# Optimization experiments

Measured on AMD Instinct MI355X. Metric: run time of the kernel, lower is better.

The kernel has to match this reference:

```python
import math
import jax, jax.numpy as jnp
import numpy as np

D_MODEL = 512
NHEAD = 8
D_HEAD = D_MODEL // NHEAD
ATTN_TEMP = 1.0
B, LQ, LK = 2, 2048, 4096


def _linear_params(key, d_in, d_out):
    kw, kb = jax.random.split(key)
    bound = 1.0 / math.sqrt(d_in)
    W = jax.random.uniform(kw, (d_out, d_in), jnp.float32, -bound, bound)
    b = jax.random.uniform(kb, (d_out,), jnp.float32, -bound, bound)
    return W, b


def setup_inputs() -> dict:
    key = jax.random.key(0)
    ks = jax.random.split(key, 8)
    q = jax.random.normal(ks[0], (B, LQ, D_MODEL), jnp.float32)
    kv = jax.random.normal(ks[1], (B, LK, D_MODEL), jnp.float32)
    key_gate = jax.random.uniform(ks[2], (B, LK), jnp.float32)
    key_mask = jax.random.randint(ks[3], (B, LK), 0, 2, jnp.int32)
    Wq, bq = _linear_params(ks[4], D_MODEL, D_MODEL)
    Wk, bk = _linear_params(ks[5], D_MODEL, D_MODEL)
    Wv, bv = _linear_params(ks[6], D_MODEL, D_MODEL)
    Wo, bo = _linear_params(ks[7], D_MODEL, D_MODEL)
    return {"q": q, "kv": kv, "key_gate": key_gate, "key_mask": key_mask,
            "Wq": Wq, "bq": bq, "Wk": Wk, "bk": bk,
            "Wv": Wv, "bv": bv, "Wo": Wo, "bo": bo}


def reference(q, kv, key_gate, key_mask, Wq, bq, Wk, bk, Wv, bv, Wo, bo):
    Bq, Lq, _ = q.shape
    _, Lk, _ = kv.shape
    # projections -> (B, H, L, Dh)
    qp = (q @ Wq.T + bq).reshape(Bq, Lq, NHEAD, D_HEAD).transpose(0, 2, 1, 3)
    kp = (kv @ Wk.T + bk).reshape(Bq, Lk, NHEAD, D_HEAD).transpose(0, 2, 1, 3)
    vp = (kv @ Wv.T + bv).reshape(Bq, Lk, NHEAD, D_HEAD).transpose(0, 2, 1, 3)
    # scores: (B, H, Lq, Lk)
    scores = jnp.einsum('bhqd,bhkd->bhqk', qp, kp) / (math.sqrt(D_HEAD) * ATTN_TEMP)
    log_gate = jnp.log(jnp.clip(key_gate, 1e-6, None))  # (B, Lk)
    scores = scores + log_gate[:, None, None, :]
    pad = (key_mask == 0)[:, None, None, :]
    scores = jnp.where(pad, -jnp.inf, scores)
    attn = jax.nn.softmax(scores, axis=-1)  # dropout is identity in eval
    out = jnp.einsum('bhqk,bhkd->bhqd', attn, vp)
    out = out.transpose(0, 2, 1, 3).reshape(Bq, Lq, D_MODEL)
    return out @ Wo.T + bo
```

## Files before the change

kernel.cpp:

```cpp
#include <hip/hip_runtime.h>
#include <hip/hip_bf16.h>


using bf16  = __hip_bfloat16;
using bf16x8 = __attribute__((ext_vector_type(8))) short;
using f32x4  = __attribute__((ext_vector_type(4))) float;

#define MFMA16(a, b, c) __builtin_amdgcn_mfma_f32_16x16x32_bf16((a), (b), (c), 0, 0, 0)

#define SCALE_LOG2E 0.18033688011112042f

__device__ __forceinline__ bf16x8 load8(const bf16* p) {
    return *reinterpret_cast<const bf16x8*>(p);
}
__device__ __forceinline__ short f2bf(float x) {
    bf16 h = __float2bfloat16(x);
    return *reinterpret_cast<short*>(&h);
}
__device__ __forceinline__ short f2bf_fast(float x) {
    unsigned u = (__builtin_bit_cast(unsigned, x) + 0x8000u) >> 16;
    return (short)u;
}
__device__ __forceinline__ float bfb2f(short s) {
    unsigned int u = ((unsigned int)(unsigned short)s) << 16;
    return __builtin_bit_cast(float, u);
}

__global__ void prep_all(const float* __restrict__ q, const float* __restrict__ kv,
                         const float* __restrict__ Wq, const float* __restrict__ Wk,
                         const float* __restrict__ Wv, const float* __restrict__ Wo,
                         const float* __restrict__ gate, const int* __restrict__ mask,
                         bf16* __restrict__ qb, bf16* __restrict__ kvb,
                         bf16* __restrict__ Wqb, bf16* __restrict__ Wkb,
                         bf16* __restrict__ Wvb, bf16* __restrict__ Wob,
                         float* __restrict__ g2) {
    const int bid = blockIdx.x;
    const int tid = threadIdx.x;
    if (bid < 7168) {
        const float* src; bf16* dst; int j;
        if (bid < 6144) {
            int i = bid * 256 + tid;
            if (i < 524288) { src = q;  dst = qb;  j = i; }
            else            { src = kv; dst = kvb; j = i - 524288; }
        } else {
            int i = (bid - 6144) * 256 + tid;
            int t = i >> 16; j = i & 65535;
            src = (t == 0) ? Wq : (t == 1) ? Wk : (t == 2) ? Wv : Wo;
            dst = (t == 0) ? Wqb : (t == 1) ? Wkb : (t == 2) ? Wvb : Wob;
        }
        float4 v = reinterpret_cast<const float4*>(src)[j];
        ushort4 o;
        o.x = (unsigned short)f2bf(v.x);
        o.y = (unsigned short)f2bf(v.y);
        o.z = (unsigned short)f2bf(v.z);
        o.w = (unsigned short)f2bf(v.w);
        reinterpret_cast<ushort4*>(dst)[j] = o;
    } else {
        int i = (bid - 7168) * 256 + tid;
        float gv = fmaxf(gate[i], 1e-6f);
        g2[i] = mask[i] ? log2f(gv) : -1e30f;
    }
}

__device__ __forceinline__ void proj_body(const bf16* __restrict__ X,
                                          const bf16* __restrict__ W,
                                          const float* __restrict__ bias,
                                          void* __restrict__ Cout,
                                          int mode, int L, int mb, bf16* Ws) {
    const int tid  = threadIdx.x;
    const int wave = tid >> 6;
    const int lane = tid & 63;
    const int li   = lane & 15;
    const int quad = lane >> 4;
    const int n0   = blockIdx.x * 64;
    const int m0   = mb * 128 + wave * 32;

    f32x4 zero = {0.f, 0.f, 0.f, 0.f};
    f32x4 acc[2][4];
    for (int mt = 0; mt < 2; ++mt)
        for (int t = 0; t < 4; ++t) acc[mt][t] = zero;

    const bf16* x0 = X + (size_t)(m0 + li) * 512;
    const bf16* x1 = X + (size_t)(m0 + 16 + li) * 512;

    for (int p = 0; p < 2; ++p) {
        __syncthreads();
        for (int i = 0; i < 8; ++i) {
            const int c  = i * 256 + tid;
            const int cr = c >> 5;
            const int kc = (c & 31) * 8;
            *reinterpret_cast<bf16x8*>(&Ws[cr * 264 + kc]) =
                load8(W + (size_t)(n0 + cr) * 512 + p * 256 + kc);
        }
        __syncthreads();

        for (int k0 = 0; k0 < 256; k0 += 32) {
            bf16x8 a0 = load8(x0 + p * 256 + k0 + quad * 8);
            bf16x8 a1 = load8(x1 + p * 256 + k0 + quad * 8);
            for (int t = 0; t < 4; ++t) {
                bf16x8 w8 = load8(&Ws[(t * 16 + li) * 264 + k0 + quad * 8]);
                acc[0][t] = MFMA16(a0, w8, acc[0][t]);
                acc[1][t] = MFMA16(a1, w8, acc[1][t]);
            }
        }
    }

    for (int t = 0; t < 4; ++t) {
        const int col = n0 + t * 16 + li;
        const float bcol = bias[col];
        for (int mt = 0; mt < 2; ++mt) {
            for (int r = 0; r < 4; ++r) {
                const int row = m0 + mt * 16 + quad * 4 + r;
                const float v = acc[mt][t][r] + bcol;
                if (mode == 0) {
                    ((float*)Cout)[(size_t)row * 512 + col] = v;
                } else {
                    const int bb2 = row / L;
                    const int i   = row - bb2 * L;
                    const int hh  = col >> 6;
                    const int dh  = col & 63;
                    size_t idx;
                    if (mode == 1) idx = ((size_t)(bb2 * 8 + hh) * L + i) * 64 + dh;
                    else           idx = ((size_t)(bb2 * 8 + hh) * 64 + dh) * L + i;
                    ((bf16*)Cout)[idx] = __float2bfloat16(v);
                }
            }
        }
    }
}

__global__ void __launch_bounds__(256, 4)
proj_qkv(const bf16* __restrict__ qb, const bf16* __restrict__ kvb,
         const bf16* __restrict__ Wq, const float* __restrict__ bq,
         const bf16* __restrict__ Wk, const float* __restrict__ bk,
         const bf16* __restrict__ Wv, const float* __restrict__ bv,
         bf16* __restrict__ qp, bf16* __restrict__ kp,
         bf16* __restrict__ vpt) {
    __shared__ alignas(16) bf16 Ws[64 * 264];
    const int my = blockIdx.y;
    if (my < 32)      proj_body(qb,  Wq, bq, qp,  1, 2048, my,      Ws);
    else if (my < 96) proj_body(kvb, Wk, bk, kp,  1, 4096, my - 32, Ws);
    else              proj_body(kvb, Wv, bv, vpt, 2, 4096, my - 96, Ws);
}

__global__ void __launch_bounds__(256, 4)
proj_o(const bf16* __restrict__ op, const bf16* __restrict__ Wo,
       const float* __restrict__ bo, float* __restrict__ out) {
    __shared__ alignas(16) bf16 Ws[64 * 264];
    proj_body(op, Wo, bo, out, 0, 1, blockIdx.y, Ws);
}

#define PS  72
#define PTS 68
__global__ void attn_kernel(const bf16* __restrict__ qp, const bf16* __restrict__ kp,
                            const bf16* __restrict__ vpt, const float* __restrict__ g2,
                            bf16* __restrict__ Opart, float* __restrict__ lpart) {
    __shared__ alignas(16) bf16 Kt[64 * PS];
    __shared__ alignas(16) bf16 Vt[64 * PS];
    __shared__ alignas(16) short Pt[4 * 32 * PTS];
    __shared__ float gs[64];

    const int tid  = threadIdx.x;
    const int wave = tid >> 6;
    const int lane = tid & 63;
    const int li   = lane & 15;
    const int quad = lane >> 4;

    const int bx = blockIdx.x;
    const int ks = bx & 3;
    const int qt = (bx >> 2) & 15;
    const int h  = (bx >> 6) & 7;
    const int b  = bx >> 9;
    const size_t bh = (size_t)(b * 8 + h);

    const bf16* qb0 = qp + (bh * 2048 + (size_t)qt * 128 + wave * 32 + li) * 64;
    bf16x8 aq[2][2];
    aq[0][0] = load8(qb0 + quad * 8);
    aq[0][1] = load8(qb0 + 32 + quad * 8);
    aq[1][0] = load8(qb0 + 16 * 64 + quad * 8);
    aq[1][1] = load8(qb0 + 16 * 64 + 32 + quad * 8);

    f32x4 zero = {0.f, 0.f, 0.f, 0.f};
    f32x4 o[2][4];
    for (int mt = 0; mt < 2; ++mt)
        for (int t = 0; t < 4; ++t) o[mt][t] = zero;
    float lsum[2][4] = {{0.f, 0.f, 0.f, 0.f}, {0.f, 0.f, 0.f, 0.f}};

    const bf16* ksrc  = kp  + bh * 4096 * 64;
    const bf16* vsrc  = vpt + bh * 64 * 4096;
    const float* gsrc = g2 + (size_t)b * 4096;

    short* PtW = &Pt[wave * 32 * PTS];
    const int r0 = tid >> 3;
    const int cg = (tid & 7) * 8;

    for (int kt = ks * 16; kt < ks * 16 + 16; ++kt) {
        {
            const bf16* kst = ksrc + (size_t)kt * 4096;
            *reinterpret_cast<bf16x8*>(&Kt[r0 * PS + cg])        = load8(kst + r0 * 64 + cg);
            *reinterpret_cast<bf16x8*>(&Kt[(r0 + 32) * PS + cg]) = load8(kst + (r0 + 32) * 64 + cg);
            const bf16* vs = vsrc + kt * 64;
            *reinterpret_cast<bf16x8*>(&Vt[r0 * PS + cg])        = load8(vs + (size_t)r0 * 4096 + cg);
            *reinterpret_cast<bf16x8*>(&Vt[(r0 + 32) * PS + cg]) = load8(vs + (size_t)(r0 + 32) * 4096 + cg);
            if (tid < 64) gs[tid] = gsrc[kt * 64 + tid];
        }
        __syncthreads();

        for (int t = 0; t < 4; ++t) {
            bf16x8 bk0 = load8(&Kt[(t * 16 + li) * PS + quad * 8]);
            bf16x8 bk1 = load8(&Kt[(t * 16 + li) * PS + 32 + quad * 8]);
            const float gv = gs[t * 16 + li];
            for (int mt = 0; mt < 2; ++mt) {
                f32x4 acc = zero;
                acc = MFMA16(aq[mt][0], bk0, acc);
                acc = MFMA16(aq[mt][1], bk1, acc);
                for (int r = 0; r < 4; ++r) {
                    const float p = __builtin_amdgcn_exp2f(fmaf(acc[r], SCALE_LOG2E, gv));
                    lsum[mt][r] += p;
                    PtW[(mt * 16 + quad * 4 + r) * PTS + t * 16 + li] = f2bf_fast(p);
                }
            }
        }

        bf16x8 ap[2][2];
        ap[0][0] = *reinterpret_cast<bf16x8*>(&PtW[li * PTS + quad * 8]);
        ap[0][1] = *reinterpret_cast<bf16x8*>(&PtW[li * PTS + 32 + quad * 8]);
        ap[1][0] = *reinterpret_cast<bf16x8*>(&PtW[(16 + li) * PTS + quad * 8]);
        ap[1][1] = *reinterpret_cast<bf16x8*>(&PtW[(16 + li) * PTS + 32 + quad * 8]);
        for (int t = 0; t < 4; ++t) {
            bf16x8 bv0 = load8(&Vt[(t * 16 + li) * PS + quad * 8]);
            bf16x8 bv1 = load8(&Vt[(t * 16 + li) * PS + 32 + quad * 8]);
            for (int mt = 0; mt < 2; ++mt) {
                o[mt][t] = MFMA16(ap[mt][0], bv0, o[mt][t]);
                o[mt][t] = MFMA16(ap[mt][1], bv1, o[mt][t]);
            }
        }
        __syncthreads();
    }

    for (int off = 1; off < 16; off <<= 1)
        for (int mt = 0; mt < 2; ++mt)
            for (int r = 0; r < 4; ++r)
                lsum[mt][r] += __shfl_xor(lsum[mt][r], off);

    bf16* ob = Opart + ((size_t)bx * 128 + wave * 32) * 64;
    for (int mt = 0; mt < 2; ++mt)
        for (int t = 0; t < 4; ++t)
            for (int r = 0; r < 4; ++r)
                ob[(size_t)(mt * 16 + quad * 4 + r) * 64 + t * 16 + li] =
                    __float2bfloat16(o[mt][t][r]);
    if (li == 0)
        for (int mt = 0; mt < 2; ++mt)
            for (int r = 0; r < 4; ++r)
                lpart[(size_t)bx * 128 + wave * 32 + mt * 16 + quad * 4 + r] = lsum[mt][r];
}

__global__ void attn_combine(const bf16* __restrict__ Opart,
                             const float* __restrict__ lpart,
                             bf16* __restrict__ op) {
    const int gidx = blockIdx.x * 256 + threadIdx.x;
    const int row  = gidx >> 2;
    const int c0   = (gidx & 3) * 16;
    const int b    = row >> 14;
    const int h    = (row >> 11) & 7;
    const int q    = row & 2047;
    const int qt   = q >> 7;
    const int r128 = q & 127;
    const int base = (((b * 8 + h) * 16) + qt) * 4;

    float acc[16];
    for (int j = 0; j < 16; ++j) acc[j] = 0.f;
    float L = 0.f;
    for (int s = 0; s < 4; ++s) {
        const bf16* src = Opart + ((size_t)(base + s) * 128 + r128) * 64 + c0;
        bf16x8 v0 = load8(src);
        bf16x8 v1 = load8(src + 8);
        for (int j = 0; j < 8; ++j) {
            acc[j]     += bfb2f(v0[j]);
            acc[8 + j] += bfb2f(v1[j]);
        }
        L += lpart[(size_t)(base + s) * 128 + r128];
    }
    const float invL = 1.0f / L;

    bf16* dst = op + ((size_t)b * 2048 + q) * 512 + h * 64 + c0;
    bf16x8 o0, o1;
    for (int j = 0; j < 8; ++j) {
        o0[j] = f2bf(acc[j] * invL);
        o1[j] = f2bf(acc[8 + j] * invL);
    }
    *reinterpret_cast<bf16x8*>(dst)     = o0;
    *reinterpret_cast<bf16x8*>(dst + 8) = o1;
}

extern "C" void kernel_launch(void* const* d_in, const int* in_sizes, int n_in,
                              void* d_out, int out_size, void* d_ws, size_t ws_size,
                              hipStream_t stream) {
    const float* q    = (const float*)d_in[0];
    const float* kv   = (const float*)d_in[1];
    const float* gate = (const float*)d_in[2];
    const int*   mask = (const int*)d_in[3];
    const float* Wq = (const float*)d_in[4];  const float* bq = (const float*)d_in[5];
    const float* Wk = (const float*)d_in[6];  const float* bk = (const float*)d_in[7];
    const float* Wv = (const float*)d_in[8];  const float* bv = (const float*)d_in[9];
    const float* Wo = (const float*)d_in[10]; const float* bo = (const float*)d_in[11];
    float* out = (float*)d_out;

    char* ws = (char*)d_ws;
    float* g2  = (float*)ws;
    bf16* Wqb  = (bf16*)(ws + (1u  << 20));
    bf16* Wkb  = (bf16*)(ws + (1u  << 20) + (512u << 10));
    bf16* Wvb  = (bf16*)(ws + (2u  << 20));
    bf16* Wob  = (bf16*)(ws + (2u  << 20) + (512u << 10));
    bf16* qb   = (bf16*)(ws + (3u  << 20));
    bf16* kvb  = (bf16*)(ws + (7u  << 20));
    bf16* qp   = (bf16*)(ws + (15u << 20));
    bf16* kp   = (bf16*)(ws + (19u << 20));
    bf16* vpt  = (bf16*)(ws + (27u << 20));
    bf16* op   = (bf16*)(ws + (35u << 20));
    bf16* Opart = (bf16*)(ws + (39u << 20));
    float* lpart = (float*)(ws + (55u << 20));

    prep_all<<<7200, 256, 0, stream>>>(q, kv, Wq, Wk, Wv, Wo, gate, mask,
                                       qb, kvb, Wqb, Wkb, Wvb, Wob, g2);
    proj_qkv<<<dim3(8, 160), 256, 0, stream>>>(qb, kvb, Wqb, bq, Wkb, bk,
                                               Wvb, bv, qp, kp, vpt);
    attn_kernel<<<1024, 256, 0, stream>>>(qp, kp, vpt, g2, Opart, lpart);
    attn_combine<<<512, 256, 0, stream>>>(Opart, lpart, op);
    proj_o<<<dim3(8, 32), 256, 0, stream>>>(op, Wob, bo, out);
}
```

Before: 217.6 us.

## Double-buffer attention K/V tiles with async global-to-LDS loads and XOR swizzle

The attention kernel now prefetches the next K/V/gate tile into a second LDS buffer using global_load_lds direct copies, so loads overlap compute. It uses an XOR swizzle instead of row padding to avoid bank conflicts, and drops the trailing barrier. The projection kernels also halve their weight LDS tile (K chunks of 128) and raise the launch-bounds occupancy hint to 8. The risks are correctness of async load ordering without explicit waits (relying on __syncthreads) and more barrier rounds in the projection.

After: 232.4 us. 6.8% more time.

```diff
diff --git a/kernel.cpp b/kernel.cpp
--- a/kernel.cpp
+++ b/kernel.cpp
@@ -24,6 +24,17 @@
 __device__ __forceinline__ float bfb2f(short s) {
     unsigned int u = ((unsigned int)(unsigned short)s) << 16;
     return __builtin_bit_cast(float, u);
+}
+
+__device__ __forceinline__ void async16(const bf16* g, bf16* l) {
+    __builtin_amdgcn_global_load_lds(
+        (const __attribute__((address_space(1))) void*)g,
+        (__attribute__((address_space(3))) void*)l, 16, 0, 0);
+}
+__device__ __forceinline__ void async4(const float* g, float* l) {
+    __builtin_amdgcn_global_load_lds(
+        (const __attribute__((address_space(1))) void*)g,
+        (__attribute__((address_space(3))) void*)l, 4, 0, 0);
 }
 
 __global__ void prep_all(const float* __restrict__ q, const float* __restrict__ kv,
@@ -83,22 +94,22 @@
     const bf16* x0 = X + (size_t)(m0 + li) * 512;
     const bf16* x1 = X + (size_t)(m0 + 16 + li) * 512;
 
-    for (int p = 0; p < 2; ++p) {
+    for (int p = 0; p < 4; ++p) {
         __syncthreads();
-        for (int i = 0; i < 8; ++i) {
-            const int c  = i * 256 + tid;
-            const int cr = c >> 5;
-            const int kc = (c & 31) * 8;
-            *reinterpret_cast<bf16x8*>(&Ws[cr * 264 + kc]) =
-                load8(W + (size_t)(n0 + cr) * 512 + p * 256 + kc);
+        for (int i = 0; i < 4; ++i) {
+            const int slot = i * 256 + tid;
+            const int row  = slot >> 4;
+            const int g    = slot & 15;
+            *reinterpret_cast<bf16x8*>(&Ws[row * 136 + g * 8]) =
+                load8(W + (size_t)(n0 + row) * 512 + p * 128 + g * 8);
         }
         __syncthreads();
 
-        for (int k0 = 0; k0 < 256; k0 += 32) {
-            bf16x8 a0 = load8(x0 + p * 256 + k0 + quad * 8);
-            bf16x8 a1 = load8(x1 + p * 256 + k0 + quad * 8);
+        for (int k0 = 0; k0 < 128; k0 += 32) {
+            bf16x8 a0 = load8(x0 + p * 128 + k0 + quad * 8);
+            bf16x8 a1 = load8(x1 + p * 128 + k0 + quad * 8);
             for (int t = 0; t < 4; ++t) {
-                bf16x8 w8 = load8(&Ws[(t * 16 + li) * 264 + k0 + quad * 8]);
+                bf16x8 w8 = load8(&Ws[(t * 16 + li) * 136 + k0 + quad * 8]);
                 acc[0][t] = MFMA16(a0, w8, acc[0][t]);
                 acc[1][t] = MFMA16(a1, w8, acc[1][t]);
             }
@@ -129,36 +140,35 @@
     }
 }
 
-__global__ void __launch_bounds__(256, 4)
+__global__ void __launch_bounds__(256, 8)
 proj_qkv(const bf16* __restrict__ qb, const bf16* __restrict__ kvb,
          const bf16* __restrict__ Wq, const float* __restrict__ bq,
          const bf16* __restrict__ Wk, const float* __restrict__ bk,
          const bf16* __restrict__ Wv, const float* __restrict__ bv,
          bf16* __restrict__ qp, bf16* __restrict__ kp,
          bf16* __restrict__ vpt) {
-    __shared__ alignas(16) bf16 Ws[64 * 264];
+    __shared__ alignas(16) bf16 Ws[64 * 136];
     const int my = blockIdx.y;
     if (my < 32)      proj_body(qb,  Wq, bq, qp,  1, 2048, my,      Ws);
     else if (my < 96) proj_body(kvb, Wk, bk, kp,  1, 4096, my - 32, Ws);
     else              proj_body(kvb, Wv, bv, vpt, 2, 4096, my - 96, Ws);
 }
 
-__global__ void __launch_bounds__(256, 4)
+__global__ void __launch_bounds__(256, 8)
 proj_o(const bf16* __restrict__ op, const bf16* __restrict__ Wo,
        const float* __restrict__ bo, float* __restrict__ out) {
-    __shared__ alignas(16) bf16 Ws[64 * 264];
+    __shared__ alignas(16) bf16 Ws[64 * 136];
     proj_body(op, Wo, bo, out, 0, 1, blockIdx.y, Ws);
 }
 
-#define PS  72
 #define PTS 68
 __global__ void attn_kernel(const bf16* __restrict__ qp, const bf16* __restrict__ kp,
                             const bf16* __restrict__ vpt, const float* __restrict__ g2,
                             bf16* __restrict__ Opart, float* __restrict__ lpart) {
-    __shared__ alignas(16) bf16 Kt[64 * PS];
-    __shared__ alignas(16) bf16 Vt[64 * PS];
+    __shared__ alignas(16) bf16 Kt[2][64 * 64];
+    __shared__ alignas(16) bf16 Vt[2][64 * 64];
     __shared__ alignas(16) short Pt[4 * 32 * PTS];
-    __shared__ float gs[64];
+    __shared__ float gs[2][64];
 
     const int tid  = threadIdx.x;
     const int wave = tid >> 6;
@@ -191,25 +201,35 @@
     const float* gsrc = g2 + (size_t)b * 4096;
 
     short* PtW = &Pt[wave * 32 * PTS];
-    const int r0 = tid >> 3;
-    const int cg = (tid & 7) * 8;
-
-    for (int kt = ks * 16; kt < ks * 16 + 16; ++kt) {
-        {
-            const bf16* kst = ksrc + (size_t)kt * 4096;
-            *reinterpret_cast<bf16x8*>(&Kt[r0 * PS + cg])        = load8(kst + r0 * 64 + cg);
-            *reinterpret_cast<bf16x8*>(&Kt[(r0 + 32) * PS + cg]) = load8(kst + (r0 + 32) * 64 + cg);
-            const bf16* vs = vsrc + kt * 64;
-            *reinterpret_cast<bf16x8*>(&Vt[r0 * PS + cg])        = load8(vs + (size_t)r0 * 4096 + cg);
-            *reinterpret_cast<bf16x8*>(&Vt[(r0 + 32) * PS + cg]) = load8(vs + (size_t)(r0 + 32) * 4096 + cg);
-            if (tid < 64) gs[tid] = gsrc[kt * 64 + tid];
-        }
+
+    const int rDMA = lane >> 3;
+    const int cDMA = ((lane & 7) ^ rDMA) << 3;
+    const int rA = wave * 16 + rDMA;
+    const int rB = rA + 8;
+
+    auto issue = [&](int kt, int buf) {
+        const bf16* kst = ksrc + (size_t)kt * 4096;
+        const bf16* vst = vsrc + kt * 64;
+        async16(kst + rA * 64 + cDMA, &Kt[buf][wave * 1024]);
+        async16(kst + rB * 64 + cDMA, &Kt[buf][wave * 1024 + 512]);
+        async16(vst + (size_t)rA * 4096 + cDMA, &Vt[buf][wave * 1024]);
+        async16(vst + (size_t)rB * 4096 + cDMA, &Vt[buf][wave * 1024 + 512]);
+        if (wave == 0) async4(gsrc + kt * 64 + lane, &gs[buf][0]);
+    };
+
+    issue(ks * 16, 0);
+
+    for (int i = 0; i < 16; ++i) {
+        const int cur = i & 1;
         __syncthreads();
+        if (i < 15) issue(ks * 16 + i + 1, cur ^ 1);
 
         for (int t = 0; t < 4; ++t) {
-            bf16x8 bk0 = load8(&Kt[(t * 16 + li) * PS + quad * 8]);
-            bf16x8 bk1 = load8(&Kt[(t * 16 + li) * PS + 32 + quad * 8]);
-            const float gv = gs[t * 16 + li];
+            const int R   = t * 16 + li;
+            const int rsw = R & 7;
+            bf16x8 bk0 = load8(&Kt[cur][R * 64 + ((quad ^ rsw) << 3)]);
+            bf16x8 bk1 = load8(&Kt[cur][R * 64 + (((4 + quad) ^ rsw) << 3)]);
+            const float gv = gs[cur][R];
             for (int mt = 0; mt < 2; ++mt) {
                 f32x4 acc = zero;
                 acc = MFMA16(aq[mt][0], bk0, acc);
@@ -228,14 +248,15 @@
         ap[1][0] = *reinterpret_cast<bf16x8*>(&PtW[(16 + li) * PTS + quad * 8]);
         ap[1][1] = *reinterpret_cast<bf16x8*>(&PtW[(16 + li) * PTS + 32 + quad * 8]);
         for (int t = 0; t < 4; ++t) {
-            bf16x8 bv0 = load8(&Vt[(t * 16 + li) * PS + quad * 8]);
-            bf16x8 bv1 = load8(&Vt[(t * 16 + li) * PS + 32 + quad * 8]);
+            const int R   = t * 16 + li;
+            const int rsw = R & 7;
+            bf16x8 bv0 = load8(&Vt[cur][R * 64 + ((quad ^ rsw) << 3)]);
+            bf16x8 bv1 = load8(&Vt[cur][R * 64 + (((4 + quad) ^ rsw) << 3)]);
             for (int mt = 0; mt < 2; ++mt) {
                 o[mt][t] = MFMA16(ap[mt][0], bv0, o[mt][t]);
                 o[mt][t] = MFMA16(ap[mt][1], bv1, o[mt][t]);
             }
         }
-        __syncthreads();
     }
 
     for (int off = 1; off < 16; off <<= 1)
```
